# Kernel optimization log

Measured on AMD Instinct MI355X. Metric: run time of the kernel, lower is better.

Reference implementation:

```python
import jax, jax.numpy as jnp
import numpy as np

TEMPERATURE = 0.03


def setup_inputs() -> dict:
    key = jax.random.key(0)
    k1, k2, k3 = jax.random.split(key, 3)
    B, d = 8192, 256
    z_a = jax.random.normal(k1, (B, d), dtype=jnp.float32)
    z_t = jax.random.normal(k2, (B, d), dtype=jnp.float32)
    # module expects L2-normalized projections
    z_a = z_a / jnp.linalg.norm(z_a, axis=-1, keepdims=True)
    z_t = z_t / jnp.linalg.norm(z_t, axis=-1, keepdims=True)
    patient_ids = jax.random.randint(k3, (B,), 0, 2048, dtype=jnp.int64)
    return {"z_a": z_a, "z_t": z_t, "patient_ids": patient_ids}


def _direction_loss(sim, cross_mask):
    # sim: (B, B) row i = anchor i vs all candidates; cross_mask: (B, B) valid negatives
    B = sim.shape[0]
    pos = jnp.diagonal(sim)                              # (B,) positive logits
    logit_mask = cross_mask | jnp.eye(B, dtype=bool)     # negatives + the positive
    lse = jax.nn.logsumexp(sim, axis=1, where=logit_mask)  # (B,)
    row_loss = lse - pos                                 # CE with label = positive
    valid = cross_mask.any(axis=1)                       # rows with >=1 cross-patient neg
    cnt = jnp.sum(valid)
    total = jnp.sum(jnp.where(valid, row_loss, 0.0))
    return jnp.where(cnt > 0, total / jnp.maximum(cnt, 1).astype(sim.dtype), 0.0)


def reference(z_a, z_t, patient_ids):
    sim = jnp.matmul(z_a, z_t.T) / TEMPERATURE           # (B, B)
    cross = patient_ids[:, None] != patient_ids[None, :] # cross-patient negative mask
    loss_a2t = _direction_loss(sim, cross)
    loss_t2a = _direction_loss(sim.T, cross.T)
    return (loss_a2t + loss_t2a) / 2.0
```

## Files before the change

kernel.cpp:

```cpp
#include <hip/hip_runtime.h>
#include <math.h>

#define BSZ    8192
#define DDIM   256
#define SCALE  33.33333333333333f
#define C_OFF  34.0f
#define SC_L2E 48.08983470f
#define C2     49.05163139f

typedef float floatx4  __attribute__((ext_vector_type(4)));
typedef float floatx16 __attribute__((ext_vector_type(16)));
typedef int   intx4    __attribute__((ext_vector_type(4)));
typedef int   intx8    __attribute__((ext_vector_type(8)));
typedef long long fp8x8;

__device__ __forceinline__ fp8x8 cvt8_f8(const float* __restrict__ g)
{
    const float4 lo = *(const float4*)g;
    const float4 hi = *(const float4*)(g + 4);
    int a = __builtin_amdgcn_cvt_pk_fp8_f32(lo.x, lo.y, 0, false);
    a     = __builtin_amdgcn_cvt_pk_fp8_f32(lo.z, lo.w, a, true);
    int b = __builtin_amdgcn_cvt_pk_fp8_f32(hi.x, hi.y, 0, false);
    b     = __builtin_amdgcn_cvt_pk_fp8_f32(hi.z, hi.w, b, true);
    int2 r; r.x = a; r.y = b;
    return *(fp8x8*)&r;
}

__global__ __launch_bounds__(256) void prep_kernel(
    const float* __restrict__ za, const float* __restrict__ zt,
    unsigned char* __restrict__ za_f8, unsigned char* __restrict__ zt_perm,
    float* __restrict__ zbase)
{
    const int bid = blockIdx.x, tid = threadIdx.x;
    if (bid < 1024) {
        const int i = (bid * 256 + tid) * 8;
        *(fp8x8*)(za_f8 + i) = cvt8_f8(za + i);
        if (bid < 16) {
            const int z = bid * 1024 + tid * 4;
            *(float4*)&zbase[z] = (float4){0.f, 0.f, 0.f, 0.f};
            if (bid == 0 && tid == 0) {
                zbase[16384] = 0.f;
                ((int*)zbase)[16385] = 0;
                ((int*)zbase)[16386] = 0;
            }
        }
    } else {
        const int S    = (bid - 1024) * 256 + tid;
        const int cbb  = S >> 12;
        const int col  = (S >> 5) & 127;
        const int gph  = (S >> 1) & 15;
        const int off8 = (S & 1) * 8;
        const int k    = ((gph ^ (col & 15)) << 4) + off8;
        const float* src = zt + (size_t)(cbb * 128 + col) * DDIM + k;
        *(fp8x8*)(zt_perm + (size_t)S * 8) = cvt8_f8(src);
    }
}

__global__ __launch_bounds__(256, 2) void sim_fused(
    const unsigned char* __restrict__ za_f8, const unsigned char* __restrict__ zt_perm,
    const int* __restrict__ pid,
    float* __restrict__ s_row, float* __restrict__ s_col,
    float* __restrict__ posv)
{
    __shared__ __align__(16) unsigned char Bs[32768];
    __shared__ int   pidc[128];
    __shared__ float colsum[128];

    const int bid   = blockIdx.x;
    const int cbb   = bid & 63, band = bid >> 6;
    const int row0  = band * 128, col0g = cbb * 128;
    const int tid   = threadIdx.x, lane = tid & 63, wid = tid >> 6;
    const int l31   = lane & 31, h = lane >> 5;
    const int rbase = row0 + wid * 32;

    if (tid < 128) { pidc[tid] = pid[col0g + tid]; colsum[tid] = 0.f; }

    {
        const unsigned char* src = zt_perm + (size_t)cbb * 32768 + wid * 8192 + lane * 16;
        unsigned char* dst = Bs + wid * 8192 + lane * 16;
        #pragma unroll
        for (int i = 0; i < 8; i++)
            __builtin_amdgcn_global_load_lds(
                (const __attribute__((address_space(1))) void*)(src + i * 1024),
                (__attribute__((address_space(3))) void*)(dst + i * 1024),
                16, 0, 0);
    }

    intx8 af[4];
    {
        const unsigned char* ga = za_f8 + (size_t)(rbase + l31) * DDIM + h * 32;
        #pragma unroll
        for (int ks = 0; ks < 4; ks++)
            af[ks] = *(const intx8*)(ga + ks * 64);
    }

    int prw[16];
    #pragma unroll
    for (int reg = 0; reg < 16; reg++)
        prw[reg] = pid[rbase + (reg & 3) + 8 * (reg >> 2) + 4 * h];

    __syncthreads();

    const int t16 = ((((lane >> 4) & 2) ^ (lane & 15)) << 4);
    int dsb[4];
    #pragma unroll
    for (int n = 0; n < 4; n++)
        dsb[n] = n * 8192 + l31 * 256 + t16;

    floatx16 acc[4];
    #pragma unroll
    for (int n = 0; n < 4; n++) acc[n] = (floatx16)0.0f;

    #pragma unroll
    for (int ks = 0; ks < 4; ks++) {
        #pragma unroll
        for (int n = 0; n < 4; n++) {
            intx4 lo = *(const intx4*)(Bs + (dsb[n] ^ (((ks * 4 + 0)) << 4)));
            intx4 hi = *(const intx4*)(Bs + (dsb[n] ^ (((ks * 4 + 1)) << 4)));
            intx8 b;
            b[0] = lo[0]; b[1] = lo[1]; b[2] = lo[2]; b[3] = lo[3];
            b[4] = hi[0]; b[5] = hi[1]; b[6] = hi[2]; b[7] = hi[3];
            acc[n] = __builtin_amdgcn_mfma_scale_f32_32x32x64_f8f6f4(
                af[ks], b, acc[n], 0, 0, 0, 0x7F7F7F7F, 0, 0x7F7F7F7F);
        }
    }

    int pc[4];
    #pragma unroll
    for (int n = 0; n < 4; n++) pc[n] = pidc[n * 32 + l31];

    float rowp[16];
    #pragma unroll
    for (int i = 0; i < 16; i++) rowp[i] = 0.f;
    float colp4[4] = {0.f, 0.f, 0.f, 0.f};

    const bool diagblk = (band == cbb);
    const int  target  = (lane & 3) + 4 * ((lane >> 3) & 3);
    const bool ownl    = (h == ((lane >> 2) & 1));

    #pragma unroll
    for (int n = 0; n < 4; n++) {
        const int pcn = pc[n];
        #pragma unroll
        for (int reg = 0; reg < 16; reg++) {
            float e = __builtin_amdgcn_exp2f(fmaf(acc[n][reg], SC_L2E, -C2));
            e = (prw[reg] != pcn) ? e : 0.f;
            colp4[n] += e;
            rowp[reg] += e;
        }
        if (diagblk && n == wid) {
            float vd = 0.f;
            #pragma unroll
            for (int reg = 0; reg < 16; reg++)
                vd = (reg == target) ? acc[n][reg] : vd;
            float ed = __builtin_amdgcn_exp2f(fmaf(vd, SC_L2E, -C2));
            ed = ownl ? ed : 0.f;
            colp4[n] += ed;
            #pragma unroll
            for (int reg = 0; reg < 16; reg++)
                rowp[reg] += (reg == target) ? ed : 0.f;
            if (ownl) posv[row0 + wid * 32 + l31] = vd * SCALE;
        }
    }

    #pragma unroll
    for (int n = 0; n < 4; n++)
        colp4[n] += __shfl_xor(colp4[n], 32, 64);
    if (lane < 32) {
        #pragma unroll
        for (int n = 0; n < 4; n++)
            atomicAdd(&colsum[n * 32 + lane], colp4[n]);
    }

#define RED(bit, c)                                                        \
    _Pragma("unroll")                                                      \
    for (int _i = 0; _i < (c); _i++) {                                     \
        float _s = (lane & (bit)) ? rowp[_i] : rowp[_i + (c)];             \
        float _o = __shfl_xor(_s, (bit), 64);                              \
        rowp[_i] = ((lane & (bit)) ? rowp[_i + (c)] : rowp[_i]) + _o;      \
    }
    RED(1, 8) RED(2, 4) RED(4, 2) RED(8, 1)
#undef RED
    rowp[0] += __shfl_xor(rowp[0], 16, 64);
    if ((lane & 16) == 0) {
        const int reg = ((lane & 1) << 3) | ((lane & 2) << 1)
                      | ((lane & 4) >> 1) | ((lane & 8) >> 3);
        const int rl  = (reg & 3) + 8 * (reg >> 2) + 4 * h;
        atomicAdd(&s_row[rbase + rl], rowp[0]);
    }

    __syncthreads();
    if (tid < 128) atomicAdd(&s_col[col0g + tid], colsum[tid]);
}

__global__ __launch_bounds__(256) void finalize_rows(
    const int* __restrict__ pid,
    const float* __restrict__ s_row, const float* __restrict__ s_col,
    const float* __restrict__ posv,
    float* __restrict__ total, int* __restrict__ flag, int* __restrict__ cnt,
    float* __restrict__ out)
{
    const int i = blockIdx.x * 256 + threadIdx.x;
    const float p = posv[i];
    const float c = (logf(s_row[i]) + C_OFF - p)
                  + (logf(s_col[i]) + C_OFF - p);

    float v = c;
    #pragma unroll
    for (int off = 32; off > 0; off >>= 1) v += __shfl_down(v, off, 64);
    if ((threadIdx.x & 63) == 0) atomicAdd(total, v);

    const unsigned long long m = __ballot(pid[i] != pid[0]);
    if (m != 0ull && (threadIdx.x & 63) == 0) atomicOr(flag, 1);

    __syncthreads();
    __threadfence();
    if (threadIdx.x == 0) {
        const int done = atomicAdd(cnt, 1);
        if (done == (int)gridDim.x - 1) {
            const float t = atomicAdd(total, 0.0f);
            const int   f = atomicOr(flag, 0);
            out[0] = f ? t / (2.0f * (float)BSZ) : 0.0f;
        }
    }
}

extern "C" void kernel_launch(void* const* d_in, const int* in_sizes, int n_in,
                              void* d_out, int out_size, void* d_ws, size_t ws_size,
                              hipStream_t stream)
{
    const float* za  = (const float*)d_in[0];
    const float* zt  = (const float*)d_in[1];
    const int*   pid = (const int*)d_in[2];
    float* out = (float*)d_out;

    unsigned char* za_f8   = (unsigned char*)d_ws;
    unsigned char* zt_perm = za_f8 + (size_t)BSZ * DDIM;
    float*  s_row   = (float*)(zt_perm + (size_t)BSZ * DDIM);
    float*  s_col   = s_row + BSZ;
    float*  total   = s_col + BSZ;
    int*    flag    = (int*)(total + 1);
    int*    cnt     = flag + 1;
    float*  posv    = (float*)(cnt + 1);

    prep_kernel<<<dim3(2048), 256, 0, stream>>>(za, zt, za_f8, zt_perm, s_row);

    sim_fused<<<dim3(4096), 256, 0, stream>>>(za_f8, zt_perm, pid,
                                              s_row, s_col, posv);

    finalize_rows<<<dim3(BSZ / 256), 256, 0, stream>>>(
        pid, s_row, s_col, posv, total, flag, cnt, out);
}
```

Baseline: 120.3 us.

## Process eight row bands per block to reuse staged column tile

```diff
diff --git a/kernel.cpp b/kernel.cpp
--- a/kernel.cpp
+++ b/kernel.cpp
@@ -67,11 +67,11 @@
     __shared__ float colsum[128];
 
     const int bid   = blockIdx.x;
-    const int cbb   = bid & 63, band = bid >> 6;
-    const int row0  = band * 128, col0g = cbb * 128;
+    const int cbb   = bid & 63;
+    const int bgrp  = bid >> 6;
+    const int col0g = cbb * 128;
     const int tid   = threadIdx.x, lane = tid & 63, wid = tid >> 6;
     const int l31   = lane & 31, h = lane >> 5;
-    const int rbase = row0 + wid * 32;
 
     if (tid < 128) { pidc[tid] = pid[col0g + tid]; colsum[tid] = 0.f; }
 
@@ -86,18 +86,15 @@
                 16, 0, 0);
     }
 
-    intx8 af[4];
+    const int band0 = bgrp * 8;
+    intx8 afc[4];
     {
-        const unsigned char* ga = za_f8 + (size_t)(rbase + l31) * DDIM + h * 32;
+        const unsigned char* ga =
+            za_f8 + (size_t)(band0 * 128 + wid * 32 + l31) * DDIM + h * 32;
         #pragma unroll
         for (int ks = 0; ks < 4; ks++)
-            af[ks] = *(const intx8*)(ga + ks * 64);
-    }
-
-    int prw[16];
-    #pragma unroll
-    for (int reg = 0; reg < 16; reg++)
-        prw[reg] = pid[rbase + (reg & 3) + 8 * (reg >> 2) + 4 * h];
+            afc[ks] = *(const intx8*)(ga + ks * 64);
+    }
 
     __syncthreads();
 
@@ -107,59 +104,100 @@
     for (int n = 0; n < 4; n++)
         dsb[n] = n * 8192 + l31 * 256 + t16;
 
-    floatx16 acc[4];
-    #pragma unroll
-    for (int n = 0; n < 4; n++) acc[n] = (floatx16)0.0f;
-
-    #pragma unroll
-    for (int ks = 0; ks < 4; ks++) {
+    int pc[4];
+    #pragma unroll
+    for (int n = 0; n < 4; n++) pc[n] = pidc[n * 32 + l31];
+
+    float colp4[4] = {0.f, 0.f, 0.f, 0.f};
+    const int  target = (lane & 3) + 4 * ((lane >> 3) & 3);
+    const bool ownl   = (h == ((lane >> 2) & 1));
+
+    #pragma unroll
+    for (int i = 0; i < 8; i++) {
+        const int band  = band0 + i;
+        const int rbase = band * 128 + wid * 32;
+
+        intx8 afn[4];
+        if (i < 7) {
+            const unsigned char* ga =
+                za_f8 + (size_t)(rbase + 128 + l31) * DDIM + h * 32;
+            #pragma unroll
+            for (int ks = 0; ks < 4; ks++)
+                afn[ks] = *(const intx8*)(ga + ks * 64);
+        }
+
+        int prw[16];
+        #pragma unroll
+        for (int reg = 0; reg < 16; reg++)
+            prw[reg] = pid[rbase + (reg & 3) + 8 * (reg >> 2) + 4 * h];
+
+        floatx16 acc[4];
+        #pragma unroll
+        for (int n = 0; n < 4; n++) acc[n] = (floatx16)0.0f;
+
+        #pragma unroll
+        for (int ks = 0; ks < 4; ks++) {
+            #pragma unroll
+            for (int n = 0; n < 4; n++) {
+                intx4 lo = *(const intx4*)(Bs + (dsb[n] ^ ((ks * 4 + 0) << 4)));
+                intx4 hi = *(const intx4*)(Bs + (dsb[n] ^ ((ks * 4 + 1) << 4)));
+                intx8 b;
+                b[0] = lo[0]; b[1] = lo[1]; b[2] = lo[2]; b[3] = lo[3];
+                b[4] = hi[0]; b[5] = hi[1]; b[6] = hi[2]; b[7] = hi[3];
+                acc[n] = __builtin_amdgcn_mfma_scale_f32_32x32x64_f8f6f4(
+                    afc[ks], b, acc[n], 0, 0, 0, 0x7F7F7F7F, 0, 0x7F7F7F7F);
+            }
+        }
+
+        float rowp[16];
+        #pragma unroll
+        for (int r = 0; r < 16; r++) rowp[r] = 0.f;
+
         #pragma unroll
         for (int n = 0; n < 4; n++) {
-            intx4 lo = *(const intx4*)(Bs + (dsb[n] ^ (((ks * 4 + 0)) << 4)));
-            intx4 hi = *(const intx4*)(Bs + (dsb[n] ^ (((ks * 4 + 1)) << 4)));
-            intx8 b;
-            b[0] = lo[0]; b[1] = lo[1]; b[2] = lo[2]; b[3] = lo[3];
-            b[4] = hi[0]; b[5] = hi[1]; b[6] = hi[2]; b[7] = hi[3];
-            acc[n] = __builtin_amdgcn_mfma_scale_f32_32x32x64_f8f6f4(
-                af[ks], b, acc[n], 0, 0, 0, 0x7F7F7F7F, 0, 0x7F7F7F7F);
-        }
-    }
-
-    int pc[4];
-    #pragma unroll
-    for (int n = 0; n < 4; n++) pc[n] = pidc[n * 32 + l31];
-
-    float rowp[16];
-    #pragma unroll
-    for (int i = 0; i < 16; i++) rowp[i] = 0.f;
-    float colp4[4] = {0.f, 0.f, 0.f, 0.f};
-
-    const bool diagblk = (band == cbb);
-    const int  target  = (lane & 3) + 4 * ((lane >> 3) & 3);
-    const bool ownl    = (h == ((lane >> 2) & 1));
-
-    #pragma unroll
-    for (int n = 0; n < 4; n++) {
-        const int pcn = pc[n];
-        #pragma unroll
-        for (int reg = 0; reg < 16; reg++) {
-            float e = __builtin_amdgcn_exp2f(fmaf(acc[n][reg], SC_L2E, -C2));
-            e = (prw[reg] != pcn) ? e : 0.f;
-            colp4[n] += e;
-            rowp[reg] += e;
-        }
-        if (diagblk && n == wid) {
-            float vd = 0.f;
-            #pragma unroll
-            for (int reg = 0; reg < 16; reg++)
-                vd = (reg == target) ? acc[n][reg] : vd;
-            float ed = __builtin_amdgcn_exp2f(fmaf(vd, SC_L2E, -C2));
-            ed = ownl ? ed : 0.f;
-            colp4[n] += ed;
-            #pragma unroll
-            for (int reg = 0; reg < 16; reg++)
-                rowp[reg] += (reg == target) ? ed : 0.f;
-            if (ownl) posv[row0 + wid * 32 + l31] = vd * SCALE;
+            const int pcn = pc[n];
+            #pragma unroll
+            for (int reg = 0; reg < 16; reg++) {
+                float e = __builtin_amdgcn_exp2f(fmaf(acc[n][reg], SC_L2E, -C2));
+                e = (prw[reg] != pcn) ? e : 0.f;
+                colp4[n] += e;
+                rowp[reg] += e;
+            }
+            if (band == cbb && n == wid) {
+                float vd = 0.f;
+                #pragma unroll
+                for (int reg = 0; reg < 16; reg++)
+                    vd = (reg == target) ? acc[n][reg] : vd;
+                float ed = __builtin_amdgcn_exp2f(fmaf(vd, SC_L2E, -C2));
+                ed = ownl ? ed : 0.f;
+                colp4[n] += ed;
+                #pragma unroll
+                for (int reg = 0; reg < 16; reg++)
+                    rowp[reg] += (reg == target) ? ed : 0.f;
+                if (ownl) posv[band * 128 + wid * 32 + l31] = vd * SCALE;
+            }
+        }
+
+#define RED(bit, c)                                                        \
+        _Pragma("unroll")                                                  \
+        for (int _i = 0; _i < (c); _i++) {                                 \
+            float _s = (lane & (bit)) ? rowp[_i] : rowp[_i + (c)];         \
+            float _o = __shfl_xor(_s, (bit), 64);                          \
+            rowp[_i] = ((lane & (bit)) ? rowp[_i + (c)] : rowp[_i]) + _o;  \
+        }
+        RED(1, 8) RED(2, 4) RED(4, 2) RED(8, 1)
+#undef RED
+        rowp[0] += __shfl_xor(rowp[0], 16, 64);
+        if ((lane & 16) == 0) {
+            const int reg = ((lane & 1) << 3) | ((lane & 2) << 1)
+                          | ((lane & 4) >> 1) | ((lane & 8) >> 3);
+            const int rl  = (reg & 3) + 8 * (reg >> 2) + 4 * h;
+            atomicAdd(&s_row[rbase + rl], rowp[0]);
+        }
+
+        if (i < 7) {
+            #pragma unroll
+            for (int ks = 0; ks < 4; ks++) afc[ks] = afn[ks];
         }
     }
 
@@ -171,24 +209,6 @@
         for (int n = 0; n < 4; n++)
             atomicAdd(&colsum[n * 32 + lane], colp4[n]);
     }
-
-#define RED(bit, c)                                                        \
-    _Pragma("unroll")                                                      \
-    for (int _i = 0; _i < (c); _i++) {                                     \
-        float _s = (lane & (bit)) ? rowp[_i] : rowp[_i + (c)];             \
-        float _o = __shfl_xor(_s, (bit), 64);                              \
-        rowp[_i] = ((lane & (bit)) ? rowp[_i + (c)] : rowp[_i]) + _o;      \
-    }
-    RED(1, 8) RED(2, 4) RED(4, 2) RED(8, 1)
-#undef RED
-    rowp[0] += __shfl_xor(rowp[0], 16, 64);
-    if ((lane & 16) == 0) {
-        const int reg = ((lane & 1) << 3) | ((lane & 2) << 1)
-                      | ((lane & 4) >> 1) | ((lane & 8) >> 3);
-        const int rl  = (reg & 3) + 8 * (reg >> 2) + 4 * h;
-        atomicAdd(&s_row[rbase + rl], rowp[0]);
-    }
-
     __syncthreads();
     if (tid < 128) atomicAdd(&s_col[col0g + tid], colsum[tid]);
 }
@@ -245,8 +265,8 @@
 
     prep_kernel<<<dim3(2048), 256, 0, stream>>>(za, zt, za_f8, zt_perm, s_row);
 
-    sim_fused<<<dim3(4096), 256, 0, stream>>>(za_f8, zt_perm, pid,
-                                              s_row, s_col, posv);
+    sim_fused<<<dim3(512), 256, 0, stream>>>(za_f8, zt_perm, pid,
+                                             s_row, s_col, posv);
 
     finalize_rows<<<dim3(BSZ / 256), 256, 0, stream>>>(
         pid, s_row, s_col, posv, total, flag, cnt, out);
```

Result: faster. 102.0 us (-15.3%).
